# Performance work log

Measured on AMD Instinct MI355X. Metric: run time of the kernel, lower is better.

The kernel has to match this reference:

```python
import jax, jax.numpy as jnp
import numpy as np

MARGIN = 1.0


def setup_inputs() -> dict:
    key = jax.random.key(0)
    k1, k2 = jax.random.split(key)
    N, D = 8192, 128
    embeddings = jax.random.normal(k1, (N, D), dtype=jnp.float32)
    labels = jax.random.randint(k2, (N,), 0, 100, dtype=jnp.int64)
    return {"embeddings": embeddings, "labels": labels}


def reference(embeddings, labels):
    N = embeddings.shape[0]
    # Pairwise Euclidean distances (torch.cdist p=2) via the expanded form.
    sq = jnp.sum(embeddings * embeddings, axis=-1)  # [N]
    d2 = sq[:, None] + sq[None, :] - 2.0 * (embeddings @ embeddings.T)  # [N, N]
    d2 = jnp.maximum(d2, 0.0)
    eye = jnp.eye(N, dtype=bool)
    # Diagonal distances are never used (masked out below); replace the zero
    # under the sqrt to keep gradients finite.
    dist = jnp.sqrt(jnp.where(eye, 1.0, d2))  # [N, N]

    same = labels[:, None] == labels[None, :]
    pos_mask = same & ~eye
    neg_mask = (~same) & ~eye

    # sum_exp_i depends only on row i: one masked row reduction, reused for all pairs.
    sum_exp = jnp.sum(jnp.where(neg_mask, jnp.exp(MARGIN - dist), 0.0), axis=1)  # [N]

    # L_ij = log(sum_exp_i + sum_exp_j) + d_ij, only on positive pairs.
    L = jnp.log(sum_exp[:, None] + sum_exp[None, :]) + dist  # [N, N]
    per_pair = jnp.where(pos_mask, jax.nn.relu(L) ** 2, 0.0)
    n_pos = jnp.sum(pos_mask).astype(per_pair.dtype)
    return jnp.sum(per_pair) / n_pos / 2.0
```

## Files before the change

### kernel.cpp

```cpp
#include <hip/hip_runtime.h>
#include <hip/hip_bf16.h>


typedef __attribute__((ext_vector_type(8))) short bf16x8;
typedef __attribute__((ext_vector_type(4))) float f32x4;

__device__ __forceinline__ unsigned short f2bf(float f) {
    unsigned u = __float_as_uint(f);
    u += 0x7fffu + ((u >> 16) & 1u);
    return (unsigned short)(u >> 16);
}

__global__ void prep_kernel(const float* __restrict__ e, float* __restrict__ sq,
                            unsigned* __restrict__ ebf, int N) {
    int row = blockIdx.x;
    int lane = threadIdx.x;
    float2 v = ((const float2*)(e + (size_t)row * 128))[lane];
    float s = v.x * v.x + v.y * v.y;
    #pragma unroll
    for (int off = 1; off < 64; off <<= 1) s += __shfl_xor(s, off, 64);
    if (lane == 0) sq[row] = s;
    unsigned bits = (unsigned)f2bf(v.x) | ((unsigned)f2bf(v.y) << 16);
    ebf[(size_t)row * 64 + lane] = bits;
}

__global__ __launch_bounds__(1024) void bucket_kernel(
    const int* __restrict__ labels,
    int* __restrict__ counts_out,
    int* __restrict__ offsets_out,
    int* __restrict__ idxbuf,
    int N)
{
    __shared__ int cnt[256];
    __shared__ int off[256];
    const int tid = threadIdx.x;
    if (tid < 256) cnt[tid] = 0;
    __syncthreads();
    for (int i = tid; i < N; i += 1024)
        atomicAdd(&cnt[(unsigned)labels[i] & 255u], 1);
    __syncthreads();
    if (tid < 64) {
        int base = tid * 4;
        int c0 = cnt[base], c1 = cnt[base + 1], c2 = cnt[base + 2], c3 = cnt[base + 3];
        int s = c0 + c1 + c2 + c3;
        int v = s;
        #pragma unroll
        for (int d = 1; d < 64; d <<= 1) {
            int u = __shfl_up(v, d, 64);
            if (tid >= d) v += u;
        }
        int excl = v - s;
        off[base]     = excl;
        off[base + 1] = excl + c0;
        off[base + 2] = excl + c0 + c1;
        off[base + 3] = excl + c0 + c1 + c2;
    }
    __syncthreads();
    if (tid < 256) cnt[tid] = off[tid];
    __syncthreads();
    for (int i = tid; i < N; i += 1024) {
        int l = (unsigned)labels[i] & 255u;
        int p = atomicAdd(&cnt[l], 1);
        idxbuf[p] = i;
    }
    __syncthreads();
    if (tid < 256) {
        offsets_out[tid] = off[tid];
        counts_out[tid] = cnt[tid] - off[tid];
    }
}

__global__ __launch_bounds__(512) void pass1_kernel(
    const unsigned short* __restrict__ ebf,
    const float* __restrict__ sq,
    const int* __restrict__ labels,
    float* __restrict__ partial1,
    int N, int nCb)
{
    __shared__ __align__(16) char a_tile[128 * 128];
    __shared__ __align__(16) char b_tile[128 * 128];
    __shared__ float rowsum[128];
    __shared__ float colsum[128];

    const int tid = threadIdx.x;
    const int lane = tid & 63, wid = tid >> 6;

    const int t = blockIdx.x;
    int bi = (int)((2.f * nCb + 1.f - __builtin_amdgcn_sqrtf(
                   (2.f * nCb + 1.f) * (2.f * nCb + 1.f) - 8.f * t)) * 0.5f);
    if (bi < 0) bi = 0;
    if (bi > nCb - 1) bi = nCb - 1;
    while (bi + 1 <= nCb - 1 && (bi + 1) * (2 * nCb - bi) / 2 <= t) ++bi;
    while (bi > 0 && bi * (2 * nCb - bi + 1) / 2 > t) --bi;
    const int bj = bi + (t - bi * (2 * nCb - bi + 1) / 2);
    const bool diag = (bi == bj);
    const int brow = bi * 128, bcol = bj * 128;

    if (tid < 128) { rowsum[tid] = 0.f; colsum[tid] = 0.f; }

    const int wm = (wid >> 2) * 64, wn = (wid & 3) * 32;
    const int lhi = lane >> 4, llo = lane & 15;

    f32x4 acc[4][2];
    #pragma unroll
    for (int m = 0; m < 4; ++m)
        #pragma unroll
        for (int n = 0; n < 2; ++n)
            acc[m][n] = (f32x4){0.f, 0.f, 0.f, 0.f};

    const char* ebfB = (const char*)ebf;

    #pragma unroll
    for (int c = 0; c < 2; ++c) {
        #pragma unroll
        for (int k = 0; k < 4; ++k) {
            int s = wid * 256 + k * 64;
            int tsel = s >> 10;
            int ls = s & 1023;
            int sl = ls + lane;
            int r = sl >> 3, j = sl & 7;
            int grow = (tsel ? bcol : brow) + r;
            const void* g = ebfB + ((size_t)grow << 8) + c * 128 + ((j ^ (r & 7)) << 4);
            char* l = (tsel ? b_tile : a_tile) + ls * 16;
            __builtin_amdgcn_global_load_lds(
                (const __attribute__((address_space(1))) unsigned*)g,
                (__attribute__((address_space(3))) unsigned*)l, 16, 0, 0);
        }
        __syncthreads();

        #pragma unroll
        for (int h = 0; h < 2; ++h) {
            const int cb = h * 64 + lhi * 16;
            bf16x8 af[4], bfr[2];
            #pragma unroll
            for (int m = 0; m < 4; ++m) {
                int r = wm + m * 16 + llo;
                af[m] = *(const bf16x8*)(a_tile + r * 128 + (cb ^ ((r & 7) << 4)));
            }
            #pragma unroll
            for (int n = 0; n < 2; ++n) {
                int r = wn + n * 16 + llo;
                bfr[n] = *(const bf16x8*)(b_tile + r * 128 + (cb ^ ((r & 7) << 4)));
            }
            #pragma unroll
            for (int m = 0; m < 4; ++m)
                #pragma unroll
                for (int n = 0; n < 2; ++n)
                    acc[m][n] = __builtin_amdgcn_mfma_f32_16x16x32_bf16(af[m], bfr[n], acc[m][n], 0, 0, 0);
        }
        __syncthreads();
    }

    const int rowbase = brow + wm;
    float sqr[4][4]; int labr[4][4];
    #pragma unroll
    for (int m = 0; m < 4; ++m)
        #pragma unroll
        for (int r = 0; r < 4; ++r) {
            int row = rowbase + m * 16 + lhi * 4 + r;
            sqr[m][r] = sq[row];
            labr[m][r] = labels[row];
        }
    float sqc[2]; int labc[2];
    #pragma unroll
    for (int n = 0; n < 2; ++n) {
        int col = bcol + wn + n * 16 + llo;
        sqc[n] = sq[col];
        labc[n] = labels[col];
    }

    float wsum[4][4] = {};
    float csum[2] = {};
    #pragma unroll
    for (int m = 0; m < 4; ++m)
        #pragma unroll
        for (int n = 0; n < 2; ++n)
            #pragma unroll
            for (int r = 0; r < 4; ++r) {
                float g = acc[m][n][r];
                float d2 = fmaxf(fmaf(-2.f, g, sqr[m][r] + sqc[n]), 0.f);
                float dist = __builtin_amdgcn_sqrtf(d2);
                float w = (labr[m][r] != labc[n]) ? __expf(1.0f - dist) : 0.f;
                wsum[m][r] += w;
                csum[n] += w;
            }
    #pragma unroll
    for (int m = 0; m < 4; ++m)
        #pragma unroll
        for (int r = 0; r < 4; ++r) {
            float s = wsum[m][r];
            #pragma unroll
            for (int off = 1; off < 16; off <<= 1) s += __shfl_xor(s, off, 64);
            if (llo == 0)
                atomicAdd(&rowsum[wm + m * 16 + lhi * 4 + r], s);
        }
    if (!diag) {
        #pragma unroll
        for (int n = 0; n < 2; ++n) {
            float s = csum[n];
            s += __shfl_xor(s, 16, 64);
            s += __shfl_xor(s, 32, 64);
            if (lhi == 0)
                atomicAdd(&colsum[wn + n * 16 + llo], s);
        }
    }
    __syncthreads();
    if (tid < 128) {
        partial1[(size_t)bj * N + brow + tid] = rowsum[tid];
        if (!diag)
            partial1[(size_t)bi * N + bcol + tid] = colsum[tid];
    }
}

__global__ void reduce1_kernel(const float* __restrict__ partial1,
                               float* __restrict__ sum_exp, int N, int nCb) {
    int row = blockIdx.x * 256 + threadIdx.x;
    if (row >= N) return;
    float s = 0.f;
    for (int cb = 0; cb < nCb; ++cb) s += partial1[(size_t)cb * N + row];
    sum_exp[row] = s;
}

__global__ __launch_bounds__(256) void pass2_kernel(
    const unsigned short* __restrict__ ebf,
    const float* __restrict__ sq,
    const float* __restrict__ sum_exp,
    const int* __restrict__ idxbuf,
    const int* __restrict__ offsets,
    const int* __restrict__ counts,
    double* __restrict__ partial2,
    unsigned* __restrict__ cnt2)
{
    __shared__ __align__(16) char a_tile[128 * 128];
    __shared__ __align__(16) char b_tile[128 * 128];
    __shared__ double bsum[4];
    __shared__ unsigned bcnt[4];

    const int L = blockIdx.x;
    const int tid = threadIdx.x;
    const int lane = tid & 63, wid = tid >> 6;
    const int cnt = counts[L], offs = offsets[L];
    const int wm = (wid >> 1) * 64, wn = (wid & 1) * 64;
    const int lhi = lane >> 4, llo = lane & 15;
    const char* ebfB = (const char*)ebf;

    float lsum = 0.f; unsigned lcnt = 0;

    if (cnt > 1) {
        const int nSub = (cnt + 127) >> 7;
        for (int si = 0; si < nSub; ++si)
        for (int sj = si; sj < nSub; ++sj) {
            const int baseA = offs + si * 128, baseB = offs + sj * 128;
            const int cntA = min(128, cnt - si * 128);
            const int cntB = min(128, cnt - sj * 128);
            const float wgt = (si == sj) ? 1.f : 2.f;
            const unsigned wgtu = (si == sj) ? 1u : 2u;

            f32x4 acc[4][4];
            #pragma unroll
            for (int m = 0; m < 4; ++m)
                #pragma unroll
                for (int n = 0; n < 4; ++n)
                    acc[m][n] = (f32x4){0.f, 0.f, 0.f, 0.f};

            for (int c = 0; c < 2; ++c) {
                #pragma unroll
                for (int i2 = 0; i2 < 8; ++i2) {
                    int sl = tid + i2 * 256;
                    int tsel = sl >> 10;
                    int s = sl & 1023;
                    int r = s >> 3, j = s & 7;
                    int base = tsel ? baseB : baseA;
                    int cc = tsel ? cntB : cntA;
                    int gr = idxbuf[base + min(r, cc - 1)];
                    uint4 v = *(const uint4*)(ebfB + ((size_t)gr << 8) + c * 128 + (j << 4));
                    char* tp = tsel ? b_tile : a_tile;
                    *(uint4*)(tp + r * 128 + (((j << 4)) ^ ((r & 7) << 4))) = v;
                }
                __syncthreads();
                #pragma unroll
                for (int h = 0; h < 2; ++h) {
                    const int cb = h * 64 + lhi * 16;
                    bf16x8 af[4], bfr[4];
                    #pragma unroll
                    for (int m = 0; m < 4; ++m) {
                        int r = wm + m * 16 + llo;
                        af[m] = *(const bf16x8*)(a_tile + r * 128 + (cb ^ ((r & 7) << 4)));
                    }
                    #pragma unroll
                    for (int n = 0; n < 4; ++n) {
                        int r = wn + n * 16 + llo;
                        bfr[n] = *(const bf16x8*)(b_tile + r * 128 + (cb ^ ((r & 7) << 4)));
                    }
                    #pragma unroll
                    for (int m = 0; m < 4; ++m)
                        #pragma unroll
                        for (int n = 0; n < 4; ++n)
                            acc[m][n] = __builtin_amdgcn_mfma_f32_16x16x32_bf16(af[m], bfr[n], acc[m][n], 0, 0, 0);
                }
                __syncthreads();
            }

            int giA[4][4]; float sqA[4][4], seA[4][4]; bool vA[4][4];
            #pragma unroll
            for (int m = 0; m < 4; ++m)
                #pragma unroll
                for (int r = 0; r < 4; ++r) {
                    int lr = wm + m * 16 + lhi * 4 + r;
                    vA[m][r] = lr < cntA;
                    int gi = idxbuf[baseA + min(lr, cntA - 1)];
                    giA[m][r] = gi;
                    sqA[m][r] = sq[gi];
                    seA[m][r] = sum_exp[gi];
                }
            int gjB[4]; float sqB[4], seB[4]; bool vB[4];
            #pragma unroll
            for (int n = 0; n < 4; ++n) {
                int lc = wn + n * 16 + llo;
                vB[n] = lc < cntB;
                int gj = idxbuf[baseB + min(lc, cntB - 1)];
                gjB[n] = gj;
                sqB[n] = sq[gj];
                seB[n] = sum_exp[gj];
            }
            #pragma unroll
            for (int m = 0; m < 4; ++m)
                #pragma unroll
                for (int n = 0; n < 4; ++n)
                    #pragma unroll
                    for (int r = 0; r < 4; ++r) {
                        float g = acc[m][n][r];
                        float d2 = fmaxf(fmaf(-2.f, g, sqA[m][r] + sqB[n]), 0.f);
                        float dist = __builtin_amdgcn_sqrtf(d2);
                        bool pos = vA[m][r] && vB[n] && (giA[m][r] != gjB[n]);
                        float Lv = __logf(seA[m][r] + seB[n]) + dist;
                        Lv = fmaxf(Lv, 0.f);
                        lsum += pos ? wgt * Lv * Lv : 0.f;
                        lcnt += pos ? wgtu : 0u;
                    }
        }
    }

    #pragma unroll
    for (int off = 1; off < 64; off <<= 1) {
        lsum += __shfl_xor(lsum, off, 64);
        lcnt += __shfl_xor(lcnt, off, 64);
    }
    if (lane == 0) { bsum[wid] = (double)lsum; bcnt[wid] = lcnt; }
    __syncthreads();
    if (tid == 0) {
        partial2[L] = bsum[0] + bsum[1] + bsum[2] + bsum[3];
        cnt2[L] = bcnt[0] + bcnt[1] + bcnt[2] + bcnt[3];
    }
}

__global__ void finalize_kernel(const double* __restrict__ partial2,
                                const unsigned* __restrict__ cnt2,
                                int nT, float* __restrict__ out) {
    __shared__ double sds[4];
    __shared__ unsigned scn[4];
    int tid = threadIdx.x, lane = tid & 63, wid = tid >> 6;
    double tt = 0.0; unsigned c = 0;
    for (int i = tid; i < nT; i += 256) { tt += partial2[i]; c += cnt2[i]; }
    #pragma unroll
    for (int off = 1; off < 64; off <<= 1) {
        tt += __shfl_xor(tt, off, 64);
        c  += __shfl_xor(c, off, 64);
    }
    if (lane == 0) { sds[wid] = tt; scn[wid] = c; }
    __syncthreads();
    if (tid == 0) {
        double s = sds[0] + sds[1] + sds[2] + sds[3];
        unsigned cc = scn[0] + scn[1] + scn[2] + scn[3];
        if (cc == 0) cc = 1;
        out[0] = (float)(s / (double)cc * 0.5);
    }
}

extern "C" void kernel_launch(void* const* d_in, const int* in_sizes, int n_in,
                              void* d_out, int out_size, void* d_ws, size_t ws_size,
                              hipStream_t stream) {
    const float* e = (const float*)d_in[0];
    const int* labels = (const int*)d_in[1];
    const int N = in_sizes[1];
    const int nCb = N / 128;
    const int nT = nCb * (nCb + 1) / 2;
    const int NL = 256;

    char* ws = (char*)d_ws;
    float*    sq       = (float*)ws;
    float*    sum_exp  = (float*)(ws + 4 * (size_t)N);
    unsigned short* ebf = (unsigned short*)(ws + 8 * (size_t)N);
    char*     p        = ws + 8 * (size_t)N + 256 * (size_t)N;
    float*    partial1 = (float*)p;
    p += (size_t)nCb * N * 4;
    int*      counts   = (int*)p;      p += NL * 4;
    int*      offsets  = (int*)p;      p += NL * 4;
    p = (char*)(((size_t)p + 7) & ~(size_t)7);
    double*   partial2 = (double*)p;   p += NL * 8;
    unsigned* cnt2     = (unsigned*)p; p += NL * 4;
    int*      idxbuf   = (int*)p;

    prep_kernel<<<N, 64, 0, stream>>>(e, sq, (unsigned*)ebf, N);
    bucket_kernel<<<1, 1024, 0, stream>>>(labels, counts, offsets, idxbuf, N);
    pass1_kernel<<<nT, 512, 0, stream>>>(ebf, sq, labels, partial1, N, nCb);
    reduce1_kernel<<<(N + 255) / 256, 256, 0, stream>>>(partial1, sum_exp, N, nCb);
    pass2_kernel<<<NL, 256, 0, stream>>>(ebf, sq, sum_exp, idxbuf, offsets, counts,
                                         partial2, cnt2);
    finalize_kernel<<<1, 256, 0, stream>>>(partial2, cnt2, NL, (float*)d_out);
}
```

Baseline: 81.62 us.

## Fuse finalize into pass2, persist pass1 tiles, batch prep rows

Several changes land together. The separate finalize kernel is removed: a ticket counter, reset in bucket_kernel, lets the last pass2 block do the final reduction. pass1 becomes a grid-stride loop over triangle tiles with a fixed grid of 1040 blocks, and prep processes 8 rows per wave in 256-thread blocks instead of one 64-thread block per row. The exp(1-d) is rewritten as e*exp(-d), with the e factor applied once per row in reduce1. Together these aim to cut launch count and per-block overhead, at the cost of relying on an atomic and fence ordering for the fused finalize.

After: 112.8 us. 1.38x slower.

```diff
diff --git a/kernel.cpp b/kernel.cpp
--- a/kernel.cpp
+++ b/kernel.cpp
@@ -11,17 +11,23 @@
     return (unsigned short)(u >> 16);
 }
 
-__global__ void prep_kernel(const float* __restrict__ e, float* __restrict__ sq,
-                            unsigned* __restrict__ ebf, int N) {
-    int row = blockIdx.x;
-    int lane = threadIdx.x;
-    float2 v = ((const float2*)(e + (size_t)row * 128))[lane];
-    float s = v.x * v.x + v.y * v.y;
+__global__ __launch_bounds__(256) void prep_kernel(
+    const float* __restrict__ e, float* __restrict__ sq,
+    unsigned* __restrict__ ebf, int N) {
+    const int lane = threadIdx.x & 63, wid = threadIdx.x >> 6;
+    const int rowbase = (blockIdx.x * 4 + wid) * 8;
     #pragma unroll
-    for (int off = 1; off < 64; off <<= 1) s += __shfl_xor(s, off, 64);
-    if (lane == 0) sq[row] = s;
-    unsigned bits = (unsigned)f2bf(v.x) | ((unsigned)f2bf(v.y) << 16);
-    ebf[(size_t)row * 64 + lane] = bits;
+    for (int it = 0; it < 8; ++it) {
+        int row = rowbase + it;
+        if (row >= N) break;
+        float2 v = ((const float2*)(e + (size_t)row * 128))[lane];
+        float s = v.x * v.x + v.y * v.y;
+        #pragma unroll
+        for (int off = 1; off < 64; off <<= 1) s += __shfl_xor(s, off, 64);
+        if (lane == 0) sq[row] = s;
+        unsigned bits = (unsigned)f2bf(v.x) | ((unsigned)f2bf(v.y) << 16);
+        ebf[(size_t)row * 64 + lane] = bits;
+    }
 }
 
 __global__ __launch_bounds__(1024) void bucket_kernel(
@@ -29,11 +35,13 @@
     int* __restrict__ counts_out,
     int* __restrict__ offsets_out,
     int* __restrict__ idxbuf,
+    unsigned* __restrict__ ticket,
     int N)
 {
     __shared__ int cnt[256];
     __shared__ int off[256];
     const int tid = threadIdx.x;
+    if (tid == 0) *ticket = 0u;
     if (tid < 256) cnt[tid] = 0;
     __syncthreads();
     for (int i = tid; i < N; i += 1024)
@@ -75,7 +83,7 @@
     const float* __restrict__ sq,
     const int* __restrict__ labels,
     float* __restrict__ partial1,
-    int N, int nCb)
+    int N, int nCb, int nT)
 {
     __shared__ __align__(16) char a_tile[128 * 128];
     __shared__ __align__(16) char b_tile[128 * 128];
@@ -84,131 +92,130 @@
 
     const int tid = threadIdx.x;
     const int lane = tid & 63, wid = tid >> 6;
-
-    const int t = blockIdx.x;
-    int bi = (int)((2.f * nCb + 1.f - __builtin_amdgcn_sqrtf(
-                   (2.f * nCb + 1.f) * (2.f * nCb + 1.f) - 8.f * t)) * 0.5f);
-    if (bi < 0) bi = 0;
-    if (bi > nCb - 1) bi = nCb - 1;
-    while (bi + 1 <= nCb - 1 && (bi + 1) * (2 * nCb - bi) / 2 <= t) ++bi;
-    while (bi > 0 && bi * (2 * nCb - bi + 1) / 2 > t) --bi;
-    const int bj = bi + (t - bi * (2 * nCb - bi + 1) / 2);
-    const bool diag = (bi == bj);
-    const int brow = bi * 128, bcol = bj * 128;
-
-    if (tid < 128) { rowsum[tid] = 0.f; colsum[tid] = 0.f; }
-
     const int wm = (wid >> 2) * 64, wn = (wid & 3) * 32;
     const int lhi = lane >> 4, llo = lane & 15;
-
-    f32x4 acc[4][2];
-    #pragma unroll
-    for (int m = 0; m < 4; ++m)
-        #pragma unroll
-        for (int n = 0; n < 2; ++n)
-            acc[m][n] = (f32x4){0.f, 0.f, 0.f, 0.f};
-
     const char* ebfB = (const char*)ebf;
 
-    #pragma unroll
-    for (int c = 0; c < 2; ++c) {
-        #pragma unroll
-        for (int k = 0; k < 4; ++k) {
-            int s = wid * 256 + k * 64;
-            int tsel = s >> 10;
-            int ls = s & 1023;
-            int sl = ls + lane;
-            int r = sl >> 3, j = sl & 7;
-            int grow = (tsel ? bcol : brow) + r;
-            const void* g = ebfB + ((size_t)grow << 8) + c * 128 + ((j ^ (r & 7)) << 4);
-            char* l = (tsel ? b_tile : a_tile) + ls * 16;
-            __builtin_amdgcn_global_load_lds(
-                (const __attribute__((address_space(1))) unsigned*)g,
-                (__attribute__((address_space(3))) unsigned*)l, 16, 0, 0);
+    for (int t = blockIdx.x; t < nT; t += gridDim.x) {
+        int bi = (int)((2.f * nCb + 1.f - __builtin_amdgcn_sqrtf(
+                       (2.f * nCb + 1.f) * (2.f * nCb + 1.f) - 8.f * t)) * 0.5f);
+        if (bi < 0) bi = 0;
+        if (bi > nCb - 1) bi = nCb - 1;
+        while (bi + 1 <= nCb - 1 && (bi + 1) * (2 * nCb - bi) / 2 <= t) ++bi;
+        while (bi > 0 && bi * (2 * nCb - bi + 1) / 2 > t) --bi;
+        const int bj = bi + (t - bi * (2 * nCb - bi + 1) / 2);
+        const bool diag = (bi == bj);
+        const int brow = bi * 128, bcol = bj * 128;
+
+        if (tid < 128) { rowsum[tid] = 0.f; colsum[tid] = 0.f; }
+
+        f32x4 acc[4][2];
+        #pragma unroll
+        for (int m = 0; m < 4; ++m)
+            #pragma unroll
+            for (int n = 0; n < 2; ++n)
+                acc[m][n] = (f32x4){0.f, 0.f, 0.f, 0.f};
+
+        #pragma unroll
+        for (int c = 0; c < 2; ++c) {
+            #pragma unroll
+            for (int k = 0; k < 4; ++k) {
+                int s = wid * 256 + k * 64;
+                int tsel = s >> 10;
+                int ls = s & 1023;
+                int sl = ls + lane;
+                int r = sl >> 3, j = sl & 7;
+                int grow = (tsel ? bcol : brow) + r;
+                const void* g = ebfB + ((size_t)grow << 8) + c * 128 + ((j ^ (r & 7)) << 4);
+                char* l = (tsel ? b_tile : a_tile) + ls * 16;
+                __builtin_amdgcn_global_load_lds(
+                    (const __attribute__((address_space(1))) unsigned*)g,
+                    (__attribute__((address_space(3))) unsigned*)l, 16, 0, 0);
+            }
+            __syncthreads();
+
+            #pragma unroll
+            for (int h = 0; h < 2; ++h) {
+                const int cb = h * 64 + lhi * 16;
+                bf16x8 af[4], bfr[2];
+                #pragma unroll
+                for (int m = 0; m < 4; ++m) {
+                    int r = wm + m * 16 + llo;
+                    af[m] = *(const bf16x8*)(a_tile + r * 128 + (cb ^ ((r & 7) << 4)));
+                }
+                #pragma unroll
+                for (int n = 0; n < 2; ++n) {
+                    int r = wn + n * 16 + llo;
+                    bfr[n] = *(const bf16x8*)(b_tile + r * 128 + (cb ^ ((r & 7) << 4)));
+                }
+                #pragma unroll
+                for (int m = 0; m < 4; ++m)
+                    #pragma unroll
+                    for (int n = 0; n < 2; ++n)
+                        acc[m][n] = __builtin_amdgcn_mfma_f32_16x16x32_bf16(af[m], bfr[n], acc[m][n], 0, 0, 0);
+            }
+            __syncthreads();
+        }
+
+        const int rowbase = brow + wm;
+        float sqr[4][4]; int labr[4][4];
+        #pragma unroll
+        for (int m = 0; m < 4; ++m)
+            #pragma unroll
+            for (int r = 0; r < 4; ++r) {
+                int row = rowbase + m * 16 + lhi * 4 + r;
+                sqr[m][r] = sq[row];
+                labr[m][r] = labels[row];
+            }
+        float sqc[2]; int labc[2];
+        #pragma unroll
+        for (int n = 0; n < 2; ++n) {
+            int col = bcol + wn + n * 16 + llo;
+            sqc[n] = sq[col];
+            labc[n] = labels[col];
+        }
+
+        float wsum[4][4] = {};
+        float csum[2] = {};
+        #pragma unroll
+        for (int m = 0; m < 4; ++m)
+            #pragma unroll
+            for (int n = 0; n < 2; ++n)
+                #pragma unroll
+                for (int r = 0; r < 4; ++r) {
+                    float g = acc[m][n][r];
+                    float d2 = fmaxf(fmaf(-2.f, g, sqr[m][r] + sqc[n]), 0.f);
+                    float dist = __builtin_amdgcn_sqrtf(d2);
+                    float w = (labr[m][r] != labc[n]) ? __expf(-dist) : 0.f;
+                    wsum[m][r] += w;
+                    csum[n] += w;
+                }
+        #pragma unroll
+        for (int m = 0; m < 4; ++m)
+            #pragma unroll
+            for (int r = 0; r < 4; ++r) {
+                float s = wsum[m][r];
+                #pragma unroll
+                for (int off = 1; off < 16; off <<= 1) s += __shfl_xor(s, off, 64);
+                if (llo == 0)
+                    atomicAdd(&rowsum[wm + m * 16 + lhi * 4 + r], s);
+            }
+        if (!diag) {
+            #pragma unroll
+            for (int n = 0; n < 2; ++n) {
+                float s = csum[n];
+                s += __shfl_xor(s, 16, 64);
+                s += __shfl_xor(s, 32, 64);
+                if (lhi == 0)
+                    atomicAdd(&colsum[wn + n * 16 + llo], s);
+            }
         }
         __syncthreads();
-
-        #pragma unroll
-        for (int h = 0; h < 2; ++h) {
-            const int cb = h * 64 + lhi * 16;
-            bf16x8 af[4], bfr[2];
-            #pragma unroll
-            for (int m = 0; m < 4; ++m) {
-                int r = wm + m * 16 + llo;
-                af[m] = *(const bf16x8*)(a_tile + r * 128 + (cb ^ ((r & 7) << 4)));
-            }
-            #pragma unroll
-            for (int n = 0; n < 2; ++n) {
-                int r = wn + n * 16 + llo;
-                bfr[n] = *(const bf16x8*)(b_tile + r * 128 + (cb ^ ((r & 7) << 4)));
-            }
-            #pragma unroll
-            for (int m = 0; m < 4; ++m)
-                #pragma unroll
-                for (int n = 0; n < 2; ++n)
-                    acc[m][n] = __builtin_amdgcn_mfma_f32_16x16x32_bf16(af[m], bfr[n], acc[m][n], 0, 0, 0);
-        }
-        __syncthreads();
-    }
-
-    const int rowbase = brow + wm;
-    float sqr[4][4]; int labr[4][4];
-    #pragma unroll
-    for (int m = 0; m < 4; ++m)
-        #pragma unroll
-        for (int r = 0; r < 4; ++r) {
-            int row = rowbase + m * 16 + lhi * 4 + r;
-            sqr[m][r] = sq[row];
-            labr[m][r] = labels[row];
-        }
-    float sqc[2]; int labc[2];
-    #pragma unroll
-    for (int n = 0; n < 2; ++n) {
-        int col = bcol + wn + n * 16 + llo;
-        sqc[n] = sq[col];
-        labc[n] = labels[col];
-    }
-
-    float wsum[4][4] = {};
-    float csum[2] = {};
-    #pragma unroll
-    for (int m = 0; m < 4; ++m)
-        #pragma unroll
-        for (int n = 0; n < 2; ++n)
-            #pragma unroll
-            for (int r = 0; r < 4; ++r) {
-                float g = acc[m][n][r];
-                float d2 = fmaxf(fmaf(-2.f, g, sqr[m][r] + sqc[n]), 0.f);
-                float dist = __builtin_amdgcn_sqrtf(d2);
-                float w = (labr[m][r] != labc[n]) ? __expf(1.0f - dist) : 0.f;
-                wsum[m][r] += w;
-                csum[n] += w;
-            }
-    #pragma unroll
-    for (int m = 0; m < 4; ++m)
-        #pragma unroll
-        for (int r = 0; r < 4; ++r) {
-            float s = wsum[m][r];
-            #pragma unroll
-            for (int off = 1; off < 16; off <<= 1) s += __shfl_xor(s, off, 64);
-            if (llo == 0)
-                atomicAdd(&rowsum[wm + m * 16 + lhi * 4 + r], s);
-        }
-    if (!diag) {
-        #pragma unroll
-        for (int n = 0; n < 2; ++n) {
-            float s = csum[n];
-            s += __shfl_xor(s, 16, 64);
-            s += __shfl_xor(s, 32, 64);
-            if (lhi == 0)
-                atomicAdd(&colsum[wn + n * 16 + llo], s);
-        }
-    }
-    __syncthreads();
-    if (tid < 128) {
-        partial1[(size_t)bj * N + brow + tid] = rowsum[tid];
-        if (!diag)
-            partial1[(size_t)bi * N + bcol + tid] = colsum[tid];
+        if (tid < 128) {
+            partial1[(size_t)bj * N + brow + tid] = rowsum[tid];
+            if (!diag)
+                partial1[(size_t)bi * N + bcol + tid] = colsum[tid];
+        }
     }
 }
 
@@ -218,7 +225,7 @@
     if (row >= N) return;
     float s = 0.f;
     for (int cb = 0; cb < nCb; ++cb) s += partial1[(size_t)cb * N + row];
-    sum_exp[row] = s;
+    sum_exp[row] = s * 2.71828182845904523f;
 }
 
 __global__ __launch_bounds__(256) void pass2_kernel(
@@ -229,14 +236,18 @@
     const int* __restrict__ offsets,
     const int* __restrict__ counts,
     double* __restrict__ partial2,
-    unsigned* __restrict__ cnt2)
+    unsigned* __restrict__ cnt2,
+    unsigned* __restrict__ ticket,
+    float* __restrict__ out)
 {
     __shared__ __align__(16) char a_tile[128 * 128];
     __shared__ __align__(16) char b_tile[128 * 128];
     __shared__ double bsum[4];
     __shared__ unsigned bcnt[4];
+    __shared__ bool isLast;
 
     const int L = blockIdx.x;
+    const int NL = gridDim.x;
     const int tid = threadIdx.x;
     const int lane = tid & 63, wid = tid >> 6;
     const int cnt = counts[L], offs = offsets[L];
@@ -351,29 +362,28 @@
     if (tid == 0) {
         partial2[L] = bsum[0] + bsum[1] + bsum[2] + bsum[3];
         cnt2[L] = bcnt[0] + bcnt[1] + bcnt[2] + bcnt[3];
-    }
-}
-
-__global__ void finalize_kernel(const double* __restrict__ partial2,
-                                const unsigned* __restrict__ cnt2,
-                                int nT, float* __restrict__ out) {
-    __shared__ double sds[4];
-    __shared__ unsigned scn[4];
-    int tid = threadIdx.x, lane = tid & 63, wid = tid >> 6;
-    double tt = 0.0; unsigned c = 0;
-    for (int i = tid; i < nT; i += 256) { tt += partial2[i]; c += cnt2[i]; }
-    #pragma unroll
-    for (int off = 1; off < 64; off <<= 1) {
-        tt += __shfl_xor(tt, off, 64);
-        c  += __shfl_xor(c, off, 64);
-    }
-    if (lane == 0) { sds[wid] = tt; scn[wid] = c; }
-    __syncthreads();
-    if (tid == 0) {
-        double s = sds[0] + sds[1] + sds[2] + sds[3];
-        unsigned cc = scn[0] + scn[1] + scn[2] + scn[3];
-        if (cc == 0) cc = 1;
-        out[0] = (float)(s / (double)cc * 0.5);
+        __threadfence();
+        isLast = (atomicAdd(ticket, 1u) == (unsigned)(NL - 1));
+    }
+    __syncthreads();
+
+    if (isLast) {
+        __threadfence();
+        double tt = (tid < NL) ? partial2[tid] : 0.0;
+        unsigned c = (tid < NL) ? cnt2[tid] : 0u;
+        #pragma unroll
+        for (int off = 1; off < 64; off <<= 1) {
+            tt += __shfl_xor(tt, off, 64);
+            c  += __shfl_xor(c, off, 64);
+        }
+        if (lane == 0) { bsum[wid] = tt; bcnt[wid] = c; }
+        __syncthreads();
+        if (tid == 0) {
+            double s = bsum[0] + bsum[1] + bsum[2] + bsum[3];
+            unsigned cc = bcnt[0] + bcnt[1] + bcnt[2] + bcnt[3];
+            if (cc == 0) cc = 1;
+            out[0] = (float)(s / (double)cc * 0.5);
+        }
     }
 }
 
@@ -396,16 +406,16 @@
     p += (size_t)nCb * N * 4;
     int*      counts   = (int*)p;      p += NL * 4;
     int*      offsets  = (int*)p;      p += NL * 4;
+    unsigned* ticket   = (unsigned*)p; p += 64;
     p = (char*)(((size_t)p + 7) & ~(size_t)7);
     double*   partial2 = (double*)p;   p += NL * 8;
     unsigned* cnt2     = (unsigned*)p; p += NL * 4;
     int*      idxbuf   = (int*)p;
 
-    prep_kernel<<<N, 64, 0, stream>>>(e, sq, (unsigned*)ebf, N);
-    bucket_kernel<<<1, 1024, 0, stream>>>(labels, counts, offsets, idxbuf, N);
-    pass1_kernel<<<nT, 512, 0, stream>>>(ebf, sq, labels, partial1, N, nCb);
+    prep_kernel<<<(N + 31) / 32, 256, 0, stream>>>(e, sq, (unsigned*)ebf, N);
+    bucket_kernel<<<1, 1024, 0, stream>>>(labels, counts, offsets, idxbuf, ticket, N);
+    pass1_kernel<<<1040, 512, 0, stream>>>(ebf, sq, labels, partial1, N, nCb, nT);
     reduce1_kernel<<<(N + 255) / 256, 256, 0, stream>>>(partial1, sum_exp, N, nCb);
     pass2_kernel<<<NL, 256, 0, stream>>>(ebf, sq, sum_exp, idxbuf, offsets, counts,
-                                         partial2, cnt2);
-    finalize_kernel<<<1, 256, 0, stream>>>(partial2, cnt2, NL, (float*)d_out);
-}
+                                         partial2, cnt2, ticket, (float*)d_out);
+}
```
